# Performance work log

Measured on AMD Instinct MI355X. Metric: run time of the kernel, lower is better.

The kernel has to match this reference:

```python
import jax, jax.numpy as jnp
import numpy as np

H, V, S = 1024, 50257, 2048

def setup_inputs() -> dict:
    key = jax.random.key(0)
    ks = jax.random.split(key, 13)
    s = 0.02
    return {
        "last_output_word": jax.random.randint(ks[0], (1,), 0, V),
        "last_hidden": jax.random.normal(ks[1], (1, 1, H), dtype=jnp.float32),
        "encoder_outputs": jax.random.normal(ks[2], (S, 1, H), dtype=jnp.float32),
        "embedding": jax.random.normal(ks[3], (V, H), dtype=jnp.float32) * s,
        "attn_W": jax.random.normal(ks[4], (H, 2 * H), dtype=jnp.float32) * s,
        "attn_b": jnp.zeros((H,), dtype=jnp.float32),
        "other": jax.random.normal(ks[5], (1, H), dtype=jnp.float32) * s,
        "W_ih": jax.random.normal(ks[6], (3 * H, 2 * H), dtype=jnp.float32) * s,
        "W_hh": jax.random.normal(ks[7], (3 * H, H), dtype=jnp.float32) * s,
        "b_ih": jnp.zeros((3 * H,), dtype=jnp.float32),
        "b_hh": jnp.zeros((3 * H,), dtype=jnp.float32),
        "out_W": jax.random.normal(ks[8], (V, 2 * H), dtype=jnp.float32) * s,
        "out_b": jnp.zeros((V,), dtype=jnp.float32),
    }

def reference(last_output_word, last_hidden, encoder_outputs, embedding,
              attn_W, attn_b, other, W_ih, W_hh, b_ih, b_hh, out_W, out_b):
    h = last_hidden[-1, 0]                      # [H] top-layer hidden
    enc = encoder_outputs[:, 0, :]              # [S, H]
    # -- concat attention (vectorized over seq_len; no tanh, matches source) --
    cat = jnp.concatenate([jnp.broadcast_to(h[None, :], enc.shape), enc], axis=-1)  # [S, 2H]
    energy = cat @ attn_W.T + attn_b            # [S, H]
    scores = energy @ other[0]                  # [S]
    attn = jax.nn.softmax(scores)               # [S]
    context = attn @ enc                        # [H]
    # -- embedding (dropout = identity in eval) --
    emb = embedding[last_output_word[0]]        # [H]
    # -- single GRU step (torch gate order: r, z, n) --
    x = jnp.concatenate([emb, context])         # [2H]
    gx = W_ih @ x + b_ih                        # [3H]
    gh = W_hh @ h + b_hh                        # [3H]
    r = jax.nn.sigmoid(gx[:H] + gh[:H])
    z = jax.nn.sigmoid(gx[H:2 * H] + gh[H:2 * H])
    n = jnp.tanh(gx[2 * H:] + r * gh[2 * H:])
    h_new = (1.0 - z) * n + z * h               # [H]
    # -- output projection + log-softmax --
    logits = out_W @ jnp.concatenate([h_new, context]) + out_b   # [V]
    log_probs = jax.nn.log_softmax(logits)[None, :]              # [1, V]
    hidden = h_new[None, None, :]                                # [1, 1, H]
    attn_weights = attn[None, None, :]                           # [1, 1, S]
    return (log_probs, hidden, attn_weights)
```

## Files before the change

kernel.cpp:

```cpp
#include <hip/hip_runtime.h>
#include <math.h>

#define HD 1024
#define VD 50257
#define SD 2048
#define NVB 12565


__device__ __forceinline__ float wred(float x) {
#pragma unroll
    for (int o = 32; o; o >>= 1) x += __shfl_down(x, o, 64);
    return x;
}

__global__ __launch_bounds__(256) void k_u2(
        const float* __restrict__ attn_W, const float* __restrict__ other,
        float* __restrict__ ws) {
    const int b = blockIdx.x, t = threadIdx.x;
    const int kt = b & 3, jc = b >> 2;
    const int k = kt * 256 + t;
    const float* Wcol = attn_W + HD + k;
    const int j0 = jc * 16;
    float acc = 0.f;
#pragma unroll
    for (int j = 0; j < 16; ++j)
        acc += other[j0 + j] * Wcol[(size_t)(j0 + j) * (2 * HD)];
    atomicAdd(&ws[k], acc);
}

__global__ __launch_bounds__(256) void k_scores(
        const float* __restrict__ enc, const float* __restrict__ ws,
        float* __restrict__ scores) {
    const int row = blockIdx.x * 4 + (threadIdx.x >> 6);
    const int lane = threadIdx.x & 63;
    const float4* p = (const float4*)(enc + (size_t)row * HD);
    const float4* q = (const float4*)ws;
    float acc = 0.f;
#pragma unroll
    for (int i = lane; i < 256; i += 64) {
        float4 a = p[i], c = q[i];
        acc += a.x * c.x + a.y * c.y + a.z * c.z + a.w * c.w;
    }
    acc = wred(acc);
    if (lane == 0) scores[row] = acc;
}

__global__ __launch_bounds__(256) void k_ctx(
        const float* __restrict__ enc, const float* __restrict__ scores,
        float* __restrict__ context, float* __restrict__ dout) {
    __shared__ float sm[SD];
    __shared__ float wr[8];
    __shared__ float bc;
    const int t = threadIdx.x, lane = t & 63, wave = t >> 6;
    float lm = -INFINITY;
    for (int i = t; i < SD; i += 256) {
        float x = scores[i];
        sm[i] = x;
        lm = fmaxf(lm, x);
    }
#pragma unroll
    for (int o = 32; o; o >>= 1) lm = fmaxf(lm, __shfl_down(lm, o, 64));
    if (lane == 0) wr[wave] = lm;
    __syncthreads();
    if (t == 0) bc = fmaxf(fmaxf(wr[0], wr[1]), fmaxf(wr[2], wr[3]));
    __syncthreads();
    const float M = bc;
    float ls = 0.f;
    for (int i = t; i < SD; i += 256) ls += __expf(sm[i] - M);
#pragma unroll
    for (int o = 32; o; o >>= 1) ls += __shfl_down(ls, o, 64);
    if (lane == 0) wr[4 + wave] = ls;
    __syncthreads();
    if (t == 0) bc = wr[4] + wr[5] + wr[6] + wr[7];
    __syncthreads();
    const float inv = 1.f / bc;
    for (int i = t; i < SD; i += 256) sm[i] = __expf(sm[i] - M) * inv;
    __syncthreads();
    if (blockIdx.x == 0)
        for (int i = t; i < SD; i += 256) dout[VD + HD + i] = sm[i];
    const int rc = blockIdx.x >> 2, ct = blockIdx.x & 3;
    const int j = ct * 256 + t;
    const int r0 = rc * 64;
    float acc = 0.f;
#pragma unroll 4
    for (int r = 0; r < 64; ++r)
        acc += sm[r0 + r] * enc[(size_t)(r0 + r) * HD + j];
    atomicAdd(&context[j], acc);
}

__global__ __launch_bounds__(256) void k_big(
        const float* __restrict__ out_W, const float* __restrict__ W_ih,
        const float* __restrict__ W_hh, const float* __restrict__ b_ih,
        const float* __restrict__ b_hh, const float* __restrict__ embedding,
        const int* __restrict__ word, const float* __restrict__ h,
        float* __restrict__ ws, float* __restrict__ dout) {
    __shared__ float4 sv[256];
    const int t = threadIdx.x, lane = t & 63, wave = t >> 6;
    const float* ctx = ws + 1024;
    if (blockIdx.x < 256) {
        const int i = blockIdx.x * 4 + wave;
        const float4* e4 = (const float4*)(embedding + (size_t)word[0] * HD);
        const float4* h4 = (const float4*)h;
        const float4* c4 = (const float4*)ctx;
        float ga[3], gx[3], gh[3];
#pragma unroll
        for (int g = 0; g < 3; ++g) {
            const int row = g * HD + i;
            const float4* pa = (const float4*)(W_ih + (size_t)row * 2 * HD);
            const float4* px = pa + 256;
            const float4* ph = (const float4*)(W_hh + (size_t)row * HD);
            float a = 0.f, x = 0.f, hh = 0.f;
#pragma unroll
            for (int k = lane; k < 256; k += 64) {
                float4 w1 = pa[k], w2 = px[k], w3 = ph[k];
                float4 v1 = e4[k], v2 = c4[k], v3 = h4[k];
                a += w1.x * v1.x + w1.y * v1.y + w1.z * v1.z + w1.w * v1.w;
                x += w2.x * v2.x + w2.y * v2.y + w2.z * v2.z + w2.w * v2.w;
                hh += w3.x * v3.x + w3.y * v3.y + w3.z * v3.z + w3.w * v3.w;
            }
            ga[g] = wred(a); gx[g] = wred(x); gh[g] = wred(hh);
        }
        if (lane == 0) {
            const float r = 1.f / (1.f + __expf(-(ga[0] + gx[0] + b_ih[i] + gh[0] + b_hh[i])));
            const float z = 1.f / (1.f + __expf(-(ga[1] + gx[1] + b_ih[HD + i] + gh[1] + b_hh[HD + i])));
            const float n = tanhf(ga[2] + gx[2] + b_ih[2 * HD + i] + r * (gh[2] + b_hh[2 * HD + i]));
            const float hn = (1.f - z) * n + z * h[i];
            dout[VD + i] = hn;
            ws[4096 + i] = hn;
        }
    } else {
        sv[t] = ((const float4*)ctx)[t];
        __syncthreads();
        const int row = (blockIdx.x - 256) * 4 + wave;
        if (row >= VD) return;
        const float4* p = (const float4*)(out_W + (size_t)row * 2 * HD + HD);
        float acc = 0.f;
#pragma unroll
        for (int i = lane; i < 256; i += 64) {
            float4 a = p[i], c = sv[i];
            acc += a.x * c.x + a.y * c.y + a.z * c.z + a.w * c.w;
        }
        acc = wred(acc);
        if (lane == 0) ws[8192 + row] = acc;
    }
}

__global__ __launch_bounds__(256) void k_fin(
        const float* __restrict__ out_W, const float* __restrict__ out_b,
        float* __restrict__ ws, float* __restrict__ dout) {
    __shared__ float4 sh[256];
    __shared__ float lgt[4];
    const int t = threadIdx.x, lane = t & 63, wave = t >> 6;
    sh[t] = ((const float4*)(ws + 4096))[t];
    __syncthreads();
    const int row = blockIdx.x * 4 + wave;
    float logit = -INFINITY;
    if (row < VD) {
        const float4* p = (const float4*)(out_W + (size_t)row * 2 * HD);
        float acc = 0.f;
#pragma unroll
        for (int i = lane; i < 256; i += 64) {
            float4 a = p[i], c = sh[i];
            acc += a.x * c.x + a.y * c.y + a.z * c.z + a.w * c.w;
        }
        acc = wred(acc);
        if (lane == 0) {
            logit = acc + ws[8192 + row] + out_b[row];
            dout[row] = logit;
        }
    }
    if (lane == 0) lgt[wave] = logit;
    __syncthreads();
    if (t == 0) {
        const float m = fmaxf(fmaxf(lgt[0], lgt[1]), fmaxf(lgt[2], lgt[3]));
        float s = 0.f;
#pragma unroll
        for (int w = 0; w < 4; ++w) s += __expf(lgt[w] - m);
        ws[61440 + 2 * blockIdx.x] = m;
        ws[61440 + 2 * blockIdx.x + 1] = s;
    }
}

__global__ __launch_bounds__(256) void k_sub(
        float* __restrict__ dout, const float* __restrict__ ws) {
    __shared__ float wm[4], wsm[4];
    __shared__ float lsef;
    const int t = threadIdx.x, lane = t & 63, wave = t >> 6;
    const float* part = ws + 61440;
    float m = -INFINITY, s = 0.f;
    for (int i = t; i < NVB; i += 256) {
        float m2 = part[2 * i], s2 = part[2 * i + 1];
        float M = fmaxf(m, m2);
        s = s * __expf(m - M) + s2 * __expf(m2 - M);
        m = M;
    }
#pragma unroll
    for (int o = 32; o; o >>= 1) {
        float m2 = __shfl_down(m, o, 64), s2 = __shfl_down(s, o, 64);
        float M = fmaxf(m, m2);
        s = s * __expf(m - M) + s2 * __expf(m2 - M);
        m = M;
    }
    if (lane == 0) { wm[wave] = m; wsm[wave] = s; }
    __syncthreads();
    if (t == 0) {
        float M = wm[0], S = wsm[0];
#pragma unroll
        for (int w = 1; w < 4; ++w) {
            float M2 = fmaxf(M, wm[w]);
            S = S * __expf(M - M2) + wsm[w] * __expf(wm[w] - M2);
            M = M2;
        }
        lsef = M + logf(S);
    }
    __syncthreads();
    const int v = blockIdx.x * 256 + t;
    if (v < VD) dout[v] -= lsef;
}

extern "C" void kernel_launch(void* const* d_in, const int* in_sizes, int n_in,
                              void* d_out, int out_size, void* d_ws, size_t ws_size,
                              hipStream_t stream) {
    const int* word = (const int*)d_in[0];
    const float* h = (const float*)d_in[1];
    const float* enc = (const float*)d_in[2];
    const float* embedding = (const float*)d_in[3];
    const float* attn_W = (const float*)d_in[4];
    const float* other = (const float*)d_in[6];
    const float* W_ih = (const float*)d_in[7];
    const float* W_hh = (const float*)d_in[8];
    const float* b_ih = (const float*)d_in[9];
    const float* b_hh = (const float*)d_in[10];
    const float* out_W = (const float*)d_in[11];
    const float* out_b = (const float*)d_in[12];
    float* out = (float*)d_out;
    float* ws = (float*)d_ws;

    hipMemsetAsync(ws, 0, 2048 * sizeof(float), stream);
    k_u2<<<256, 256, 0, stream>>>(attn_W, other, ws);
    k_scores<<<512, 256, 0, stream>>>(enc, ws, ws + 2048);
    k_ctx<<<128, 256, 0, stream>>>(enc, ws + 2048, ws + 1024, out);
    k_big<<<256 + NVB, 256, 0, stream>>>(out_W, W_ih, W_hh, b_ih, b_hh,
                                         embedding, word, h, ws, out);
    k_fin<<<NVB, 256, 0, stream>>>(out_W, out_b, ws, out);
    k_sub<<<197, 256, 0, stream>>>(out, ws);
}
```

Baseline: 681.1 us.

## Fuse attention and GRU stages into one grid-barrier kernel and merge logits passes

Combines the u2, scores, softmax/context and GRU kernels into a single persistent kernel synchronized by software grid barriers. The input-independent GRU matvecs are computed alongside the attention projection instead of waiting for the context. The output projection now reads each full out_W row once in a single logits kernel rather than splitting it across two kernels with an intermediate buffer. This cuts launch count and intermediate traffic, but relies on all 512 blocks being co-resident for the spin barriers.

```diff
diff --git a/kernel.cpp b/kernel.cpp
--- a/kernel.cpp
+++ b/kernel.cpp
@@ -5,6 +5,7 @@
 #define VD 50257
 #define SD 2048
 #define NVB 12565
+#define FRONT_BLOCKS 512
 
 
 __device__ __forceinline__ float wred(float x) {
@@ -13,145 +14,161 @@
     return x;
 }
 
-__global__ __launch_bounds__(256) void k_u2(
+__device__ __forceinline__ void gbar(unsigned int* cnt, unsigned int target) {
+    __syncthreads();
+    __threadfence();
+    if (threadIdx.x == 0) {
+        __hip_atomic_fetch_add(cnt, 1u, __ATOMIC_RELEASE, __HIP_MEMORY_SCOPE_AGENT);
+        while (__hip_atomic_load(cnt, __ATOMIC_ACQUIRE, __HIP_MEMORY_SCOPE_AGENT) < target) {}
+    }
+    __syncthreads();
+    __threadfence();
+}
+
+__global__ __launch_bounds__(256) void k_front(
         const float* __restrict__ attn_W, const float* __restrict__ other,
-        float* __restrict__ ws) {
-    const int b = blockIdx.x, t = threadIdx.x;
-    const int kt = b & 3, jc = b >> 2;
-    const int k = kt * 256 + t;
-    const float* Wcol = attn_W + HD + k;
-    const int j0 = jc * 16;
-    float acc = 0.f;
-#pragma unroll
-    for (int j = 0; j < 16; ++j)
-        acc += other[j0 + j] * Wcol[(size_t)(j0 + j) * (2 * HD)];
-    atomicAdd(&ws[k], acc);
-}
-
-__global__ __launch_bounds__(256) void k_scores(
-        const float* __restrict__ enc, const float* __restrict__ ws,
-        float* __restrict__ scores) {
-    const int row = blockIdx.x * 4 + (threadIdx.x >> 6);
-    const int lane = threadIdx.x & 63;
-    const float4* p = (const float4*)(enc + (size_t)row * HD);
-    const float4* q = (const float4*)ws;
-    float acc = 0.f;
-#pragma unroll
-    for (int i = lane; i < 256; i += 64) {
-        float4 a = p[i], c = q[i];
-        acc += a.x * c.x + a.y * c.y + a.z * c.z + a.w * c.w;
-    }
-    acc = wred(acc);
-    if (lane == 0) scores[row] = acc;
-}
-
-__global__ __launch_bounds__(256) void k_ctx(
-        const float* __restrict__ enc, const float* __restrict__ scores,
-        float* __restrict__ context, float* __restrict__ dout) {
+        const float* __restrict__ enc, const float* __restrict__ embedding,
+        const int* __restrict__ word, const float* __restrict__ h,
+        const float* __restrict__ W_ih, const float* __restrict__ W_hh,
+        const float* __restrict__ b_ih, const float* __restrict__ b_hh,
+        float* __restrict__ ws, float* __restrict__ dout) {
     __shared__ float sm[SD];
     __shared__ float wr[8];
     __shared__ float bc;
-    const int t = threadIdx.x, lane = t & 63, wave = t >> 6;
-    float lm = -INFINITY;
-    for (int i = t; i < SD; i += 256) {
-        float x = scores[i];
-        sm[i] = x;
-        lm = fmaxf(lm, x);
-    }
-#pragma unroll
-    for (int o = 32; o; o >>= 1) lm = fmaxf(lm, __shfl_down(lm, o, 64));
-    if (lane == 0) wr[wave] = lm;
-    __syncthreads();
-    if (t == 0) bc = fmaxf(fmaxf(wr[0], wr[1]), fmaxf(wr[2], wr[3]));
-    __syncthreads();
-    const float M = bc;
-    float ls = 0.f;
-    for (int i = t; i < SD; i += 256) ls += __expf(sm[i] - M);
-#pragma unroll
-    for (int o = 32; o; o >>= 1) ls += __shfl_down(ls, o, 64);
-    if (lane == 0) wr[4 + wave] = ls;
-    __syncthreads();
-    if (t == 0) bc = wr[4] + wr[5] + wr[6] + wr[7];
-    __syncthreads();
-    const float inv = 1.f / bc;
-    for (int i = t; i < SD; i += 256) sm[i] = __expf(sm[i] - M) * inv;
-    __syncthreads();
-    if (blockIdx.x == 0)
-        for (int i = t; i < SD; i += 256) dout[VD + HD + i] = sm[i];
-    const int rc = blockIdx.x >> 2, ct = blockIdx.x & 3;
-    const int j = ct * 256 + t;
-    const int r0 = rc * 64;
-    float acc = 0.f;
-#pragma unroll 4
-    for (int r = 0; r < 64; ++r)
-        acc += sm[r0 + r] * enc[(size_t)(r0 + r) * HD + j];
-    atomicAdd(&context[j], acc);
-}
-
-__global__ __launch_bounds__(256) void k_big(
-        const float* __restrict__ out_W, const float* __restrict__ W_ih,
-        const float* __restrict__ W_hh, const float* __restrict__ b_ih,
-        const float* __restrict__ b_hh, const float* __restrict__ embedding,
-        const int* __restrict__ word, const float* __restrict__ h,
-        float* __restrict__ ws, float* __restrict__ dout) {
-    __shared__ float4 sv[256];
-    const int t = threadIdx.x, lane = t & 63, wave = t >> 6;
-    const float* ctx = ws + 1024;
-    if (blockIdx.x < 256) {
-        const int i = blockIdx.x * 4 + wave;
+    unsigned int* cnt = (unsigned int*)(ws + 2048);
+    float* u2 = ws;
+    float* context = ws + 1024;
+    float* scores = ws + 2304;
+    float* hnew = ws + 4352;
+    float* gA = ws + 5376;
+    float* gh = ws + 8448;
+    const int b = blockIdx.x, t = threadIdx.x;
+    const int lane = t & 63, wave = t >> 6;
+
+    if (b < 32) {
+        const int kt = b & 3, jc = b >> 2;
+        const int k = kt * 256 + t;
+        const float* Wcol = attn_W + HD + k;
+        const int j0 = jc * 128;
+        float acc = 0.f;
+#pragma unroll 8
+        for (int j = 0; j < 128; ++j)
+            acc += other[j0 + j] * Wcol[(size_t)(j0 + j) * (2 * HD)];
+        atomicAdd(&u2[k], acc);
+    } else if (b < 288) {
+        const int i = (b - 32) * 4 + wave;
         const float4* e4 = (const float4*)(embedding + (size_t)word[0] * HD);
         const float4* h4 = (const float4*)h;
-        const float4* c4 = (const float4*)ctx;
-        float ga[3], gx[3], gh[3];
 #pragma unroll
         for (int g = 0; g < 3; ++g) {
             const int row = g * HD + i;
             const float4* pa = (const float4*)(W_ih + (size_t)row * 2 * HD);
-            const float4* px = pa + 256;
             const float4* ph = (const float4*)(W_hh + (size_t)row * HD);
-            float a = 0.f, x = 0.f, hh = 0.f;
+            float a = 0.f, hh = 0.f;
 #pragma unroll
             for (int k = lane; k < 256; k += 64) {
-                float4 w1 = pa[k], w2 = px[k], w3 = ph[k];
-                float4 v1 = e4[k], v2 = c4[k], v3 = h4[k];
+                float4 w1 = pa[k], w3 = ph[k];
+                float4 v1 = e4[k], v3 = h4[k];
                 a += w1.x * v1.x + w1.y * v1.y + w1.z * v1.z + w1.w * v1.w;
-                x += w2.x * v2.x + w2.y * v2.y + w2.z * v2.z + w2.w * v2.w;
                 hh += w3.x * v3.x + w3.y * v3.y + w3.z * v3.z + w3.w * v3.w;
             }
-            ga[g] = wred(a); gx[g] = wred(x); gh[g] = wred(hh);
+            a = wred(a); hh = wred(hh);
+            if (lane == 0) {
+                gA[row] = a + b_ih[row];
+                gh[row] = hh + b_hh[row];
+            }
+        }
+    }
+    gbar(cnt + 0, FRONT_BLOCKS);
+
+    {
+        const int row = b * 4 + wave;
+        const float4* p = (const float4*)(enc + (size_t)row * HD);
+        const float4* q = (const float4*)u2;
+        float acc = 0.f;
+#pragma unroll
+        for (int i = lane; i < 256; i += 64) {
+            float4 a = p[i], c = q[i];
+            acc += a.x * c.x + a.y * c.y + a.z * c.z + a.w * c.w;
+        }
+        acc = wred(acc);
+        if (lane == 0) scores[row] = acc;
+    }
+    gbar(cnt + 1, FRONT_BLOCKS);
+
+    if (b < 128) {
+        float lm = -INFINITY;
+        for (int i = t; i < SD; i += 256) {
+            float x = scores[i];
+            sm[i] = x;
+            lm = fmaxf(lm, x);
+        }
+#pragma unroll
+        for (int o = 32; o; o >>= 1) lm = fmaxf(lm, __shfl_down(lm, o, 64));
+        if (lane == 0) wr[wave] = lm;
+        __syncthreads();
+        if (t == 0) bc = fmaxf(fmaxf(wr[0], wr[1]), fmaxf(wr[2], wr[3]));
+        __syncthreads();
+        const float M = bc;
+        float ls = 0.f;
+        for (int i = t; i < SD; i += 256) ls += __expf(sm[i] - M);
+#pragma unroll
+        for (int o = 32; o; o >>= 1) ls += __shfl_down(ls, o, 64);
+        if (lane == 0) wr[4 + wave] = ls;
+        __syncthreads();
+        if (t == 0) bc = wr[4] + wr[5] + wr[6] + wr[7];
+        __syncthreads();
+        const float inv = 1.f / bc;
+        for (int i = t; i < SD; i += 256) sm[i] = __expf(sm[i] - M) * inv;
+        __syncthreads();
+        if (b == 0)
+            for (int i = t; i < SD; i += 256) dout[VD + HD + i] = sm[i];
+        const int rc = b >> 2, ct = b & 3;
+        const int j = ct * 256 + t;
+        const int r0 = rc * 64;
+        float acc = 0.f;
+#pragma unroll 4
+        for (int r = 0; r < 64; ++r)
+            acc += sm[r0 + r] * enc[(size_t)(r0 + r) * HD + j];
+        atomicAdd(&context[j], acc);
+    }
+    gbar(cnt + 2, FRONT_BLOCKS);
+
+    if (b < 256) {
+        const int i = b * 4 + wave;
+        const float4* c4 = (const float4*)context;
+        float x2[3];
+#pragma unroll
+        for (int g = 0; g < 3; ++g) {
+            const float4* px = (const float4*)(W_ih + (size_t)(g * HD + i) * 2 * HD + HD);
+            float a = 0.f;
+#pragma unroll
+            for (int k = lane; k < 256; k += 64) {
+                float4 w = px[k], c = c4[k];
+                a += w.x * c.x + w.y * c.y + w.z * c.z + w.w * c.w;
+            }
+            x2[g] = wred(a);
         }
         if (lane == 0) {
-            const float r = 1.f / (1.f + __expf(-(ga[0] + gx[0] + b_ih[i] + gh[0] + b_hh[i])));
-            const float z = 1.f / (1.f + __expf(-(ga[1] + gx[1] + b_ih[HD + i] + gh[1] + b_hh[HD + i])));
-            const float n = tanhf(ga[2] + gx[2] + b_ih[2 * HD + i] + r * (gh[2] + b_hh[2 * HD + i]));
+            const float r = 1.f / (1.f + __expf(-(gA[i] + x2[0] + gh[i])));
+            const float z = 1.f / (1.f + __expf(-(gA[HD + i] + x2[1] + gh[HD + i])));
+            const float n = tanhf(gA[2 * HD + i] + x2[2] + r * gh[2 * HD + i]);
             const float hn = (1.f - z) * n + z * h[i];
             dout[VD + i] = hn;
-            ws[4096 + i] = hn;
-        }
-    } else {
-        sv[t] = ((const float4*)ctx)[t];
-        __syncthreads();
-        const int row = (blockIdx.x - 256) * 4 + wave;
-        if (row >= VD) return;
-        const float4* p = (const float4*)(out_W + (size_t)row * 2 * HD + HD);
-        float acc = 0.f;
-#pragma unroll
-        for (int i = lane; i < 256; i += 64) {
-            float4 a = p[i], c = sv[i];
-            acc += a.x * c.x + a.y * c.y + a.z * c.z + a.w * c.w;
-        }
-        acc = wred(acc);
-        if (lane == 0) ws[8192 + row] = acc;
-    }
-}
-
-__global__ __launch_bounds__(256) void k_fin(
+            hnew[i] = hn;
+        }
+    }
+}
+
+__global__ __launch_bounds__(256) void k_logits(
         const float* __restrict__ out_W, const float* __restrict__ out_b,
-        float* __restrict__ ws, float* __restrict__ dout) {
-    __shared__ float4 sh[256];
+        const float* __restrict__ ws, float* __restrict__ part,
+        float* __restrict__ dout) {
+    __shared__ float4 sy[512];
     __shared__ float lgt[4];
     const int t = threadIdx.x, lane = t & 63, wave = t >> 6;
-    sh[t] = ((const float4*)(ws + 4096))[t];
+    sy[t] = ((const float4*)(ws + 4352))[t];
+    sy[t + 256] = ((const float4*)(ws + 1024))[t];
     __syncthreads();
     const int row = blockIdx.x * 4 + wave;
     float logit = -INFINITY;
@@ -159,13 +176,13 @@
         const float4* p = (const float4*)(out_W + (size_t)row * 2 * HD);
         float acc = 0.f;
 #pragma unroll
-        for (int i = lane; i < 256; i += 64) {
-            float4 a = p[i], c = sh[i];
+        for (int i = lane; i < 512; i += 64) {
+            float4 a = p[i], c = sy[i];
             acc += a.x * c.x + a.y * c.y + a.z * c.z + a.w * c.w;
         }
         acc = wred(acc);
         if (lane == 0) {
-            logit = acc + ws[8192 + row] + out_b[row];
+            logit = acc + out_b[row];
             dout[row] = logit;
         }
     }
@@ -176,17 +193,16 @@
         float s = 0.f;
 #pragma unroll
         for (int w = 0; w < 4; ++w) s += __expf(lgt[w] - m);
-        ws[61440 + 2 * blockIdx.x] = m;
-        ws[61440 + 2 * blockIdx.x + 1] = s;
+        part[2 * blockIdx.x] = m;
+        part[2 * blockIdx.x + 1] = s;
     }
 }
 
 __global__ __launch_bounds__(256) void k_sub(
-        float* __restrict__ dout, const float* __restrict__ ws) {
+        float* __restrict__ dout, const float* __restrict__ part) {
     __shared__ float wm[4], wsm[4];
     __shared__ float lsef;
     const int t = threadIdx.x, lane = t & 63, wave = t >> 6;
-    const float* part = ws + 61440;
     float m = -INFINITY, s = 0.f;
     for (int i = t; i < NVB; i += 256) {
         float m2 = part[2 * i], s2 = part[2 * i + 1];
@@ -236,12 +252,9 @@
     float* out = (float*)d_out;
     float* ws = (float*)d_ws;
 
-    hipMemsetAsync(ws, 0, 2048 * sizeof(float), stream);
-    k_u2<<<256, 256, 0, stream>>>(attn_W, other, ws);
-    k_scores<<<512, 256, 0, stream>>>(enc, ws, ws + 2048);
-    k_ctx<<<128, 256, 0, stream>>>(enc, ws + 2048, ws + 1024, out);
-    k_big<<<256 + NVB, 256, 0, stream>>>(out_W, W_ih, W_hh, b_ih, b_hh,
-                                         embedding, word, h, ws, out);
-    k_fin<<<NVB, 256, 0, stream>>>(out_W, out_b, ws, out);
-    k_sub<<<197, 256, 0, stream>>>(out, ws);
-}
+    hipMemsetAsync(ws, 0, 2064 * sizeof(float), stream);
+    k_front<<<FRONT_BLOCKS, 256, 0, stream>>>(attn_W, other, enc, embedding, word,
+                                              h, W_ih, W_hh, b_ih, b_hh, ws, out);
+    k_logits<<<NVB, 256, 0, stream>>>(out_W, out_b, ws, ws + 12288, out);
+    k_sub<<<197, 256, 0, stream>>>(out, ws + 12288);
+}
```

Result: slower. 1.091 ms (+60.2%).
